# Kernel optimization log

Hardware: AMD Instinct MI355X
Metric: run time of the kernel (lower is better)

The kernel has to match this reference:

```python
import jax, jax.numpy as jnp
import numpy as np

N, R, E, H, D_MAX = 1024, 8192, 1024, 4, 48
DH = E // H
P_EDGE = 16.0 / R  # average in-degree ~16


def setup_inputs() -> dict:
    key = jax.random.key(0)
    ks = jax.random.split(key, 6)
    s = 0.02
    return {
        "target": jax.random.normal(ks[0], (N, E), jnp.float32),
        "source": jax.random.normal(ks[1], (R, E), jnp.float32),
        "adj": (jax.random.uniform(ks[2], (N, R)) < P_EDGE).astype(jnp.float32),
        "W_trans": jax.random.normal(ks[3], (E, E), jnp.float32) * s,
        "b_trans": jnp.zeros((E,), jnp.float32),
        "in_proj_w": jax.random.normal(ks[4], (3 * E, E), jnp.float32) * s,
        "in_proj_b": jnp.zeros((3 * E,), jnp.float32),
        "out_w": jax.random.normal(ks[5], (E, E), jnp.float32) * s,
        "out_b": jnp.zeros((E,), jnp.float32),
        "unit_id": 0,
    }


def reference(target, source, adj, W_trans, b_trans, in_proj_w, in_proj_b, out_w, out_b, unit_id):
    # source = relu(trans_fc(source))
    src = jax.nn.relu(source @ W_trans.T + b_trans)  # [R, E]

    # build padded neighbor index lists (torch loops per node; here vectorized)
    deg = adj.sum(axis=1).astype(jnp.int32)                # [N]
    order = jnp.argsort(-adj, axis=1)[:, :D_MAX]           # stable: 1-columns first, ascending col idx
    valid = jnp.arange(D_MAX)[None, :] < deg[:, None]      # [N, D] True = real neighbor
    neigh = jnp.where(valid, order, 0)                     # pad with index 0 (masked, like torch)
    kv_in = src[neigh]                                     # [N, D, E] gathered neighbor feats

    # nn.MultiheadAttention: q=target (len-1 query), k=v=padded neighbors
    Wq, Wk, Wv = jnp.split(in_proj_w, 3, axis=0)
    bq, bk, bv = jnp.split(in_proj_b, 3)
    q = (target @ Wq.T + bq).reshape(-1, H, DH)            # [N, H, dh]
    k = (kv_in @ Wk.T + bk).reshape(-1, D_MAX, H, DH)      # [N, D, H, dh]
    v = (kv_in @ Wv.T + bv).reshape(-1, D_MAX, H, DH)

    scores = jnp.einsum('nhd,nkhd->nhk', q, k) / np.float32(np.sqrt(DH))  # [N, H, D]
    # key_padding_mask: padded slots -> -inf; give zero-degree nodes one dummy
    # unmasked slot so softmax stays finite (their output is zeroed below)
    safe_valid = valid.at[:, 0].set(valid[:, 0] | (deg == 0))
    scores = jnp.where(safe_valid[:, None, :], scores, -jnp.inf)
    attn = jax.nn.softmax(scores, axis=-1)
    out = jnp.einsum('nhk,nkhd->nhd', attn, v).reshape(-1, E)
    out = out @ out_w.T + out_b

    # scatter back: inactive (degree-0) nodes stay zero, like att_res_padded
    return jnp.where((deg > 0)[:, None], out, jnp.zeros((), out.dtype))
```

## Files before the change

### kernel.cpp

```cpp
#include <hip/hip_runtime.h>

#define N_NODES 1024
#define R_SRC   8192
#define E_DIM   1024
#define H_HEADS 4
#define DH_DIM  256
#define D_MAXN  48
#define NCONVB  1024

typedef __attribute__((ext_vector_type(8))) short short8;
typedef __attribute__((ext_vector_type(4))) float f32x4;

__device__ __forceinline__ unsigned short f2bf(float f) {
    unsigned u = __float_as_uint(f);
    unsigned r = u + 0x7fffu + ((u >> 16) & 1u);
    return (unsigned short)(r >> 16);
}
__device__ __forceinline__ float bf2f(unsigned short b) {
    return __uint_as_float(((unsigned)b) << 16);
}
__device__ __forceinline__ void gload16(const void* g, void* l) {
    __builtin_amdgcn_global_load_lds(
        (const __attribute__((address_space(1))) unsigned int*)g,
        (__attribute__((address_space(3))) unsigned int*)l,
        16, 0, 0);
}
template<int N> __device__ __forceinline__ void vwait() {
    if constexpr (N == 8)       asm volatile("s_waitcnt vmcnt(8)" ::: "memory");
    else if constexpr (N == 6)  asm volatile("s_waitcnt vmcnt(6)" ::: "memory");
    else if constexpr (N == 4)  asm volatile("s_waitcnt vmcnt(4)" ::: "memory");
    else if constexpr (N == 2)  asm volatile("s_waitcnt vmcnt(2)" ::: "memory");
    else                        asm volatile("s_waitcnt vmcnt(0)" ::: "memory");
}

struct GD {
    const unsigned short* A;
    const unsigned short* B;
    const float* bias;
    void* C;
    int N, K, nbx, relu, outbf;
    const int* rowmask;
};

template<int BM, int BN>
__global__ __launch_bounds__(512) void gemm_t(GD d0, GD d1, int split)
{
    constexpr int AI = BM / 64;
    constexpr int BI = BN / 64;
    constexpr int VN = AI + BI;
    constexpr int FM = BM / 32;
    constexpr int FN = BN / 64;

    __shared__ __align__(16) unsigned short lds[3][(BM + BN) * 64];

    int bid = blockIdx.x;
    const int nwg = gridDim.x;
    bid = (bid & 7) * (nwg >> 3) + (bid >> 3);

    GD d; int q;
    if (bid < split) { d = d0; q = bid; }
    else             { d = d1; q = bid - split; }
    const int m0 = (q / d.nbx) * BM;
    const int n0 = (q % d.nbx) * BN;
    const int K  = d.K;

    const int t = threadIdx.x;
    const int w = t >> 6, l = t & 63;
    const int wm = w >> 2, wn = w & 3;

    const int trow = t >> 3, tkc = t & 7;
    const int tswz = tkc ^ (trow & 7);
    const unsigned short* gA[AI];
    const unsigned short* gB[BI];
#pragma unroll
    for (int i = 0; i < AI; ++i)
        gA[i] = d.A + (size_t)(m0 + i * 64 + trow) * K + tswz * 8;
#pragma unroll
    for (int i = 0; i < BI; ++i)
        gB[i] = d.B + (size_t)(n0 + i * 64 + trow) * K + tswz * 8;

    f32x4 acc[FM][FN] = {};

    auto STAGE = [&](int c, int kt) {
        const int ko = kt * 64;
#pragma unroll
        for (int i = 0; i < AI; ++i)
            gload16(gA[i] + ko, &lds[c][(i * 512 + t) * 8]);
#pragma unroll
        for (int i = 0; i < BI; ++i)
            gload16(gB[i] + ko, &lds[c][BM * 64 + (i * 512 + t) * 8]);
    };

    const int nt = K / 64;
    STAGE(0, 0);
    STAGE(1, 1);
    vwait<VN>();
    __builtin_amdgcn_s_barrier();

    const int lr = l & 15, hi = l >> 4;
    const int rsw = l & 7;
    const int cs0 = ((0 + hi) ^ rsw) * 8;
    const int cs1 = ((4 + hi) ^ rsw) * 8;
    const int abase = (wm * (BM / 2) + lr) * 64;
    const int bbase = BM * 64 + (wn * 64 + lr) * 64;

    for (int kt = 0; kt < nt; ++kt) {
        const int cur = kt % 3;
        if (kt + 2 < nt) STAGE((kt + 2) % 3, kt + 2);

        const unsigned short* Ls = &lds[cur][0];

        short8 bv[FN][2];
#pragma unroll
        for (int fj = 0; fj < FN; ++fj) {
            bv[fj][0] = *(const short8*)&Ls[bbase + fj * 1024 + cs0];
            bv[fj][1] = *(const short8*)&Ls[bbase + fj * 1024 + cs1];
        }
#pragma unroll
        for (int g = 0; g < FM; g += 4) {
            short8 av[4][2];
#pragma unroll
            for (int fi = 0; fi < 4; ++fi) {
                av[fi][0] = *(const short8*)&Ls[abase + (g + fi) * 1024 + cs0];
                av[fi][1] = *(const short8*)&Ls[abase + (g + fi) * 1024 + cs1];
            }
            __builtin_amdgcn_s_setprio(1);
#pragma unroll
            for (int ks = 0; ks < 2; ++ks)
#pragma unroll
                for (int fi = 0; fi < 4; ++fi)
#pragma unroll
                    for (int fj = 0; fj < FN; ++fj)
                        acc[g + fi][fj] = __builtin_amdgcn_mfma_f32_16x16x32_bf16(
                            av[fi][ks], bv[fj][ks], acc[g + fi][fj], 0, 0, 0);
            __builtin_amdgcn_s_setprio(0);
        }

        asm volatile("" ::: "memory");
        __builtin_amdgcn_s_barrier();
        if (kt + 2 < nt) {
            vwait<VN>();
        } else {
            vwait<0>();
        }
        __builtin_amdgcn_s_barrier();
    }

#pragma unroll
    for (int fj = 0; fj < FN; ++fj) {
        const int c = n0 + wn * 64 + fj * 16 + lr;
        const float bvs = d.bias[c];
#pragma unroll
        for (int fi = 0; fi < FM; ++fi) {
            const int rb = m0 + wm * (BM / 2) + fi * 16 + hi * 4;
#pragma unroll
            for (int qq = 0; qq < 4; ++qq) {
                const int r = rb + qq;
                float x = acc[fi][fj][qq] + bvs;
                if (d.relu) x = fmaxf(x, 0.0f);
                if (d.rowmask && d.rowmask[r] == 0) x = 0.0f;
                if (d.outbf) ((unsigned short*)d.C)[(size_t)r * d.N + c] = f2bf(x);
                else         ((float*)d.C)[(size_t)r * d.N + c] = x;
            }
        }
    }
}

struct GS {
    const unsigned short* A;
    const unsigned short* B;
    const float* bias;
    void* C;
    int lda, ldb, ldc, K, relu, outbf;
    long long azs, bzs, czs;
    int bias_zs;
    const int* rowmask;
};

__global__ __launch_bounds__(256) void gemm_s(GS g)
{
    const int z = blockIdx.z;
    const unsigned short* A = g.A + (size_t)((long long)z * g.azs);
    const unsigned short* B = g.B + (size_t)((long long)z * g.bzs);
    const float* bias = g.bias ? g.bias + (size_t)z * g.bias_zs : nullptr;

    __shared__ __align__(16) unsigned short S[3][128 * 32];

    const int t = threadIdx.x;
    const int m0 = blockIdx.y * 64;
    const int n0 = blockIdx.x * 64;
    const int w = t >> 6, l = t & 63;
    const int wrow = (w >> 1) * 32;
    const int wcol = (w & 1) * 32;
    const int lr = l & 15;
    const int kg = (l >> 4) * 8;

    f32x4 acc[2][2] = {};

    const unsigned short* gp0 = A + (size_t)(m0 + (t >> 2)) * g.lda + (t & 3) * 8;
    const unsigned short* gp1 = B + (size_t)(n0 + (t >> 2)) * g.ldb + (t & 3) * 8;

    auto STAGE = [&](int c, int k0) {
        gload16(gp0 + k0, &S[c][t * 8]);
        gload16(gp1 + k0, &S[c][2048 + t * 8]);
    };

    const int nt = g.K / 32;
    STAGE(0, 0);
    STAGE(1, 32);
    vwait<2>();
    __builtin_amdgcn_s_barrier();

    for (int kt = 0; kt < nt; ++kt) {
        const int cur = kt % 3;
        if (kt + 2 < nt) STAGE((kt + 2) % 3, (kt + 2) * 32);

        const unsigned short* Ls = &S[cur][0];

        short8 af[2], bw[2];
#pragma unroll
        for (int i = 0; i < 2; ++i)
            af[i] = *(const short8*)&Ls[(wrow + i * 16 + lr) * 32 + kg];
#pragma unroll
        for (int j = 0; j < 2; ++j)
            bw[j] = *(const short8*)&Ls[2048 + (wcol + j * 16 + lr) * 32 + kg];
#pragma unroll
        for (int i = 0; i < 2; ++i)
#pragma unroll
            for (int j = 0; j < 2; ++j)
                acc[i][j] = __builtin_amdgcn_mfma_f32_16x16x32_bf16(
                    af[i], bw[j], acc[i][j], 0, 0, 0);

        asm volatile("" ::: "memory");
        __builtin_amdgcn_s_barrier();
        if (kt + 2 < nt) {
            vwait<2>();
        } else {
            vwait<0>();
        }
        __builtin_amdgcn_s_barrier();
    }

#pragma unroll
    for (int j = 0; j < 2; ++j) {
        const int c = n0 + wcol + j * 16 + lr;
        const float bv = bias ? bias[c] : 0.0f;
#pragma unroll
        for (int i = 0; i < 2; ++i) {
            const int rbase = m0 + wrow + i * 16 + (l >> 4) * 4;
#pragma unroll
            for (int qq = 0; qq < 4; ++qq) {
                const int r = rbase + qq;
                float x = acc[i][j][qq] + bv;
                if (g.relu) x = fmaxf(x, 0.0f);
                if (g.rowmask && g.rowmask[r] == 0) x = 0.0f;
                if (g.outbf)
                    ((unsigned short*)g.C)[(size_t)((long long)z * g.czs) + (size_t)r * g.ldc + c] = f2bf(x);
                else
                    ((float*)g.C)[(size_t)((long long)z * g.czs) + (size_t)r * g.ldc + c] = x;
            }
        }
    }
}

struct ConvArgs {
    const float* s[4];
    unsigned short* d[4];
    unsigned off[5];
};

__global__ __launch_bounds__(256) void pre_kernel(
    const float* __restrict__ adj, int* __restrict__ neigh, int* __restrict__ deg,
    ConvArgs a, const float* __restrict__ inw_f, const float* __restrict__ tgt_f,
    const float* __restrict__ in_b, unsigned short* __restrict__ WkT,
    unsigned short* __restrict__ Q_bf)
{
    __shared__ __align__(16) unsigned char smem[64 * 65 * 4];
    const int t = threadIdx.x;

    if (blockIdx.x < 256) {
        unsigned short (*QS)[64 * 32] = (unsigned short (*)[64 * 32])smem;
        const int qb = blockIdx.x;
        const int m0 = (qb >> 4) * 64;
        const int n0 = (qb & 15) * 64;
        const int w = t >> 6, l = t & 63;
        const int wrow = (w >> 1) * 32;
        const int wcol = (w & 1) * 32;
        const int lr = l & 15;
        const int kg = (l >> 4) * 8;
        const int row = t >> 2, k8 = (t & 3) * 8;

        const float* ga = tgt_f + (size_t)(m0 + row) * E_DIM + k8;
        const float* gb = inw_f + (size_t)(n0 + row) * E_DIM + k8;

        f32x4 acc[2][2] = {};

        for (int k0 = 0; k0 < E_DIM; k0 += 32) {
            float4 a0 = *(const float4*)(ga + k0);
            float4 a1 = *(const float4*)(ga + k0 + 4);
            float4 b0 = *(const float4*)(gb + k0);
            float4 b1 = *(const float4*)(gb + k0 + 4);
            short8 av, bv;
            av[0] = (short)f2bf(a0.x); av[1] = (short)f2bf(a0.y);
            av[2] = (short)f2bf(a0.z); av[3] = (short)f2bf(a0.w);
            av[4] = (short)f2bf(a1.x); av[5] = (short)f2bf(a1.y);
            av[6] = (short)f2bf(a1.z); av[7] = (short)f2bf(a1.w);
            bv[0] = (short)f2bf(b0.x); bv[1] = (short)f2bf(b0.y);
            bv[2] = (short)f2bf(b0.z); bv[3] = (short)f2bf(b0.w);
            bv[4] = (short)f2bf(b1.x); bv[5] = (short)f2bf(b1.y);
            bv[6] = (short)f2bf(b1.z); bv[7] = (short)f2bf(b1.w);
            *(short8*)&QS[0][row * 32 + k8] = av;
            *(short8*)&QS[1][row * 32 + k8] = bv;
            __syncthreads();

            short8 af[2], bw[2];
#pragma unroll
            for (int i = 0; i < 2; ++i)
                af[i] = *(const short8*)&QS[0][(wrow + i * 16 + lr) * 32 + kg];
#pragma unroll
            for (int j = 0; j < 2; ++j)
                bw[j] = *(const short8*)&QS[1][(wcol + j * 16 + lr) * 32 + kg];
#pragma unroll
            for (int i = 0; i < 2; ++i)
#pragma unroll
                for (int j = 0; j < 2; ++j)
                    acc[i][j] = __builtin_amdgcn_mfma_f32_16x16x32_bf16(
                        af[i], bw[j], acc[i][j], 0, 0, 0);
            __syncthreads();
        }

#pragma unroll
        for (int j = 0; j < 2; ++j) {
            const int c = n0 + wcol + j * 16 + lr;
            const float bv = in_b[c];
#pragma unroll
            for (int i = 0; i < 2; ++i) {
                const int rbase = m0 + wrow + i * 16 + (l >> 4) * 4;
#pragma unroll
                for (int qq = 0; qq < 4; ++qq)
                    Q_bf[(size_t)(rbase + qq) * E_DIM + c] = f2bf(acc[i][j][qq] + bv);
            }
        }
        return;
    }

    if (blockIdx.x < 512) {
        float (*tile)[65] = (float (*)[65])smem;
        const int tb = blockIdx.x - 256;
        const int h = tb >> 6, rem = tb & 63;
        const int e0 = (rem >> 2) * 64, d0 = (rem & 3) * 64;
        const int r = t >> 2, c4 = (t & 3) * 16;
        const float* tsrc = inw_f + (size_t)(E_DIM + h * 256 + d0 + r) * E_DIM + e0 + c4;
#pragma unroll
        for (int jj = 0; jj < 4; ++jj) {
            float4 v = ((const float4*)tsrc)[jj];
            tile[r][c4 + jj * 4 + 0] = v.x;
            tile[r][c4 + jj * 4 + 1] = v.y;
            tile[r][c4 + jj * 4 + 2] = v.z;
            tile[r][c4 + jj * 4 + 3] = v.w;
        }
        __syncthreads();
        const int er = t >> 2, dc = (t & 3) * 16;
        unsigned short* wout = WkT + ((size_t)h * E_DIM + e0 + er) * 256 + d0 + dc;
#pragma unroll
        for (int jj = 0; jj < 4; ++jj) {
            ushort4 o;
            o.x = f2bf(tile[dc + jj * 4 + 0][er]);
            o.y = f2bf(tile[dc + jj * 4 + 1][er]);
            o.z = f2bf(tile[dc + jj * 4 + 2][er]);
            o.w = f2bf(tile[dc + jj * 4 + 3][er]);
            ((ushort4*)wout)[jj] = o;
        }
        return;
    }

    if (blockIdx.x < (unsigned)(512 + N_NODES)) {
        int* s_cnt = (int*)smem;
        int (*s_idx)[D_MAXN] = (int (*)[D_MAXN])(smem + 16);

        const int n    = blockIdx.x - 512;
        const int w    = t >> 6;
        const int lane = t & 63;
        const float* row = adj + (size_t)n * R_SRC;

        const int seg0 = w * (R_SRC / 4);
        const unsigned long long lower = (1ULL << lane) - 1ULL;
        int total = 0;

        for (int base = seg0; base < seg0 + R_SRC / 4; base += 256) {
            const float v0 = row[base + lane];
            const float v1 = row[base + 64 + lane];
            const float v2 = row[base + 128 + lane];
            const float v3 = row[base + 192 + lane];
            const unsigned long long m0 = __ballot(v0 != 0.0f);
            const unsigned long long m1 = __ballot(v1 != 0.0f);
            const unsigned long long m2 = __ballot(v2 != 0.0f);
            const unsigned long long m3 = __ballot(v3 != 0.0f);
            int p;
            p = total + __popcll(m0 & lower);
            if (v0 != 0.0f && p < D_MAXN) s_idx[w][p] = base + lane;
            total += __popcll(m0);
            p = total + __popcll(m1 & lower);
            if (v1 != 0.0f && p < D_MAXN) s_idx[w][p] = base + 64 + lane;
            total += __popcll(m1);
            p = total + __popcll(m2 & lower);
            if (v2 != 0.0f && p < D_MAXN) s_idx[w][p] = base + 128 + lane;
            total += __popcll(m2);
            p = total + __popcll(m3 & lower);
            if (v3 != 0.0f && p < D_MAXN) s_idx[w][p] = base + 192 + lane;
            total += __popcll(m3);
        }
        if (lane == 0) s_cnt[w] = total;
        __syncthreads();

        int start = 0;
#pragma unroll
        for (int i = 0; i < 4; ++i) if (i < w) start += s_cnt[i];
        const int degree = s_cnt[0] + s_cnt[1] + s_cnt[2] + s_cnt[3];
        const int nstore = total < D_MAXN ? total : D_MAXN;
        if (lane < nstore) {
            const int gpos = start + lane;
            if (gpos < D_MAXN) neigh[n * D_MAXN + gpos] = s_idx[w][lane];
        }
        if (t == 0) deg[n] = degree;
        return;
    }

    {
        const unsigned total = a.off[4];
        const unsigned stride = NCONVB * 1024;
        for (unsigned bs = (blockIdx.x - 512 - N_NODES) * 1024; bs < total; bs += stride) {
            float4 v[4];
            unsigned idx[4];
            int ok[4];
#pragma unroll
            for (int j = 0; j < 4; ++j) {
                idx[j] = bs + j * 256 + t;
                ok[j] = idx[j] < total;
            }
            int seg[4];
#pragma unroll
            for (int j = 0; j < 4; ++j) {
                seg[j] = 0;
#pragma unroll
                for (int s = 1; s < 4; ++s) seg[j] += (idx[j] >= a.off[s]);
            }
#pragma unroll
            for (int j = 0; j < 4; ++j)
                if (ok[j]) v[j] = ((const float4*)a.s[seg[j]])[idx[j] - a.off[seg[j]]];
#pragma unroll
            for (int j = 0; j < 4; ++j) {
                if (ok[j]) {
                    ushort4 o;
                    o.x = f2bf(v[j].x); o.y = f2bf(v[j].y);
                    o.z = f2bf(v[j].z); o.w = f2bf(v[j].w);
                    ((ushort4*)a.d[seg[j]])[idx[j] - a.off[seg[j]]] = o;
                }
            }
        }
    }
}

__global__ __launch_bounds__(256) void gather_ctx(
    const float* __restrict__ Ahat, const unsigned short* __restrict__ srcrel,
    const int* __restrict__ neigh, const int* __restrict__ deg,
    unsigned short* __restrict__ ctx)
{
    const int n = blockIdx.x;
    const int t = threadIdx.x;
    const int h = t >> 6;
    const int lane = t & 63;

    unsigned short* crow = ctx + ((size_t)n * H_HEADS + h) * E_DIM + lane * 16;
    const int degree = deg[n];
    if (degree == 0) {
        ushort4 z4 = {0, 0, 0, 0};
#pragma unroll
        for (int j = 0; j < 4; ++j) ((ushort4*)crow)[j] = z4;
        return;
    }
    const int dv = degree < D_MAXN ? degree : D_MAXN;

    __shared__ int s_neigh[D_MAXN];
    if (t < dv) s_neigh[t] = neigh[n * D_MAXN + t];
    __syncthreads();

    float a[16];
    {
        const float4* ap = (const float4*)(Ahat + (size_t)n * (H_HEADS * E_DIM) + h * E_DIM + lane * 16);
#pragma unroll
        for (int j = 0; j < 4; ++j) {
            float4 v = ap[j];
            a[j * 4 + 0] = v.x; a[j * 4 + 1] = v.y; a[j * 4 + 2] = v.z; a[j * 4 + 3] = v.w;
        }
    }

    float m = -3.4e38f, sum = 0.0f;
    float cacc[16];
#pragma unroll
    for (int i = 0; i < 16; ++i) cacc[i] = 0.0f;

    const float scale = 0.0625f;

    int d = 0;
    for (; d + 1 < dv; d += 2) {
        const ushort4* rp0 = (const ushort4*)(srcrel + (size_t)s_neigh[d]     * E_DIM + lane * 16);
        const ushort4* rp1 = (const ushort4*)(srcrel + (size_t)s_neigh[d + 1] * E_DIM + lane * 16);
        ushort4 w00 = rp0[0], w01 = rp0[1], w02 = rp0[2], w03 = rp0[3];
        ushort4 w10 = rp1[0], w11 = rp1[1], w12 = rp1[2], w13 = rp1[3];
        float e0[16], e1[16];
        e0[0]=bf2f(w00.x); e0[1]=bf2f(w00.y); e0[2]=bf2f(w00.z); e0[3]=bf2f(w00.w);
        e0[4]=bf2f(w01.x); e0[5]=bf2f(w01.y); e0[6]=bf2f(w01.z); e0[7]=bf2f(w01.w);
        e0[8]=bf2f(w02.x); e0[9]=bf2f(w02.y); e0[10]=bf2f(w02.z); e0[11]=bf2f(w02.w);
        e0[12]=bf2f(w03.x); e0[13]=bf2f(w03.y); e0[14]=bf2f(w03.z); e0[15]=bf2f(w03.w);
        e1[0]=bf2f(w10.x); e1[1]=bf2f(w10.y); e1[2]=bf2f(w10.z); e1[3]=bf2f(w10.w);
        e1[4]=bf2f(w11.x); e1[5]=bf2f(w11.y); e1[6]=bf2f(w11.z); e1[7]=bf2f(w11.w);
        e1[8]=bf2f(w12.x); e1[9]=bf2f(w12.y); e1[10]=bf2f(w12.z); e1[11]=bf2f(w12.w);
        e1[12]=bf2f(w13.x); e1[13]=bf2f(w13.y); e1[14]=bf2f(w13.z); e1[15]=bf2f(w13.w);

        float s0 = 0.0f, s1 = 0.0f;
#pragma unroll
        for (int i = 0; i < 16; ++i) { s0 = fmaf(a[i], e0[i], s0); s1 = fmaf(a[i], e1[i], s1); }
#pragma unroll
        for (int off = 32; off > 0; off >>= 1) {
            s0 += __shfl_xor(s0, off);
            s1 += __shfl_xor(s1, off);
        }
        s0 *= scale; s1 *= scale;

        if (s0 > m) {
            const float f = __expf(m - s0);
            sum *= f;
#pragma unroll
            for (int i = 0; i < 16; ++i) cacc[i] *= f;
            m = s0;
        }
        {
            const float wgt = __expf(s0 - m);
            sum += wgt;
#pragma unroll
            for (int i = 0; i < 16; ++i) cacc[i] = fmaf(wgt, e0[i], cacc[i]);
        }
        if (s1 > m) {
            const float f = __expf(m - s1);
            sum *= f;
#pragma unroll
            for (int i = 0; i < 16; ++i) cacc[i] *= f;
            m = s1;
        }
        {
            const float wgt = __expf(s1 - m);
            sum += wgt;
#pragma unroll
            for (int i = 0; i < 16; ++i) cacc[i] = fmaf(wgt, e1[i], cacc[i]);
        }
    }
    for (; d < dv; ++d) {
        const ushort4* rp = (const ushort4*)(srcrel + (size_t)s_neigh[d] * E_DIM + lane * 16);
        float e[16];
#pragma unroll
        for (int j = 0; j < 4; ++j) {
            ushort4 v = rp[j];
            e[j * 4 + 0] = bf2f(v.x); e[j * 4 + 1] = bf2f(v.y);
            e[j * 4 + 2] = bf2f(v.z); e[j * 4 + 3] = bf2f(v.w);
        }
        float s = 0.0f;
#pragma unroll
        for (int i = 0; i < 16; ++i) s = fmaf(a[i], e[i], s);
#pragma unroll
        for (int off = 32; off > 0; off >>= 1) s += __shfl_xor(s, off);
        s *= scale;
        if (s > m) {
            const float f = __expf(m - s);
            sum *= f;
#pragma unroll
            for (int i = 0; i < 16; ++i) cacc[i] *= f;
            m = s;
        }
        const float wgt = __expf(s - m);
        sum += wgt;
#pragma unroll
        for (int i = 0; i < 16; ++i) cacc[i] = fmaf(wgt, e[i], cacc[i]);
    }

    const float inv = 1.0f / sum;
#pragma unroll
    for (int j = 0; j < 4; ++j) {
        ushort4 o;
        o.x = f2bf(cacc[j * 4 + 0] * inv);
        o.y = f2bf(cacc[j * 4 + 1] * inv);
        o.z = f2bf(cacc[j * 4 + 2] * inv);
        o.w = f2bf(cacc[j * 4 + 3] * inv);
        ((ushort4*)crow)[j] = o;
    }
}

extern "C" void kernel_launch(void* const* d_in, const int* in_sizes, int n_in,
                              void* d_out, int out_size, void* d_ws, size_t ws_size,
                              hipStream_t stream)
{
    const float* target  = (const float*)d_in[0];
    const float* source  = (const float*)d_in[1];
    const float* adj     = (const float*)d_in[2];
    const float* W_trans = (const float*)d_in[3];
    const float* b_trans = (const float*)d_in[4];
    const float* in_w    = (const float*)d_in[5];
    const float* in_b    = (const float*)d_in[6];
    const float* out_w   = (const float*)d_in[7];
    const float* out_b   = (const float*)d_in[8];
    float* out = (float*)d_out;

    char* ws = (char*)d_ws;
    unsigned short* src_bf    = (unsigned short*)ws; ws += (size_t)R_SRC * E_DIM * 2;
    unsigned short* wt_bf     = (unsigned short*)ws; ws += (size_t)E_DIM * E_DIM * 2;
    unsigned short* wv_bf     = (unsigned short*)ws; ws += (size_t)E_DIM * E_DIM * 2;
    unsigned short* outw_bf   = (unsigned short*)ws; ws += (size_t)E_DIM * E_DIM * 2;
    unsigned short* srcrel_bf = (unsigned short*)ws; ws += (size_t)R_SRC * E_DIM * 2;
    unsigned short* WkT_bf    = (unsigned short*)ws; ws += (size_t)H_HEADS * E_DIM * DH_DIM * 2;
    unsigned short* Q_bf      = (unsigned short*)ws; ws += (size_t)N_NODES * E_DIM * 2;
    float*          Ahat      = (float*)ws;         ws += (size_t)N_NODES * H_HEADS * E_DIM * 4;
    unsigned short* ctx_bf    = (unsigned short*)ws; ws += (size_t)N_NODES * H_HEADS * E_DIM * 2;
    unsigned short* attn_bf   = (unsigned short*)ws; ws += (size_t)N_NODES * E_DIM * 2;
    int*            neigh     = (int*)ws;            ws += (size_t)N_NODES * D_MAXN * 4;
    int*            deg       = (int*)ws;            ws += (size_t)N_NODES * 4;

    const size_t EE = (size_t)E_DIM * E_DIM;

    {
        ConvArgs a;
        const unsigned sz4[4] = {
            (unsigned)((size_t)R_SRC * E_DIM / 4),
            (unsigned)(EE / 4),
            (unsigned)(EE / 4),
            (unsigned)(EE / 4)};
        a.s[0] = source;        a.d[0] = src_bf;
        a.s[1] = W_trans;       a.d[1] = wt_bf;
        a.s[2] = in_w + 2 * EE; a.d[2] = wv_bf;
        a.s[3] = out_w;         a.d[3] = outw_bf;
        a.off[0] = 0;
        for (int i = 0; i < 4; ++i) a.off[i + 1] = a.off[i] + sz4[i];
        pre_kernel<<<512 + N_NODES + NCONVB, 256, 0, stream>>>(
            adj, neigh, deg, a, in_w, target, in_b, WkT_bf, Q_bf);
    }

    {
        GD ds;
        ds.A = src_bf; ds.B = wt_bf; ds.bias = b_trans; ds.C = srcrel_bf;
        ds.N = E_DIM; ds.K = E_DIM; ds.nbx = E_DIM / 256; ds.relu = 1; ds.outbf = 1;
        ds.rowmask = nullptr;
        const int sblocks = (R_SRC / 128) * (E_DIM / 256);
        gemm_t<128, 256><<<sblocks, 512, 0, stream>>>(ds, ds, sblocks);
    }

    {
        GS g;
        g.A = Q_bf; g.B = WkT_bf; g.bias = nullptr; g.C = Ahat;
        g.lda = E_DIM; g.ldb = DH_DIM; g.ldc = H_HEADS * E_DIM; g.K = DH_DIM;
        g.relu = 0; g.outbf = 0;
        g.azs = DH_DIM;
        g.bzs = (long long)E_DIM * DH_DIM;
        g.czs = E_DIM;
        g.bias_zs = 0; g.rowmask = nullptr;
        gemm_s<<<dim3(E_DIM / 64, N_NODES / 64, H_HEADS), 256, 0, stream>>>(g);
    }

    gather_ctx<<<N_NODES, 256, 0, stream>>>(Ahat, srcrel_bf, neigh, deg, ctx_bf);

    {
        GS g;
        g.A = ctx_bf; g.B = wv_bf; g.bias = in_b + 2 * E_DIM; g.C = attn_bf;
        g.lda = H_HEADS * E_DIM; g.ldb = E_DIM; g.ldc = E_DIM; g.K = E_DIM;
        g.relu = 0; g.outbf = 1;
        g.azs = E_DIM;
        g.bzs = (long long)DH_DIM * E_DIM;
        g.czs = DH_DIM;
        g.bias_zs = DH_DIM; g.rowmask = nullptr;
        gemm_s<<<dim3(DH_DIM / 64, N_NODES / 64, H_HEADS), 256, 0, stream>>>(g);
    }

    {
        GS g;
        g.A = attn_bf; g.B = outw_bf; g.bias = out_b; g.C = out;
        g.lda = E_DIM; g.ldb = E_DIM; g.ldc = E_DIM; g.K = E_DIM;
        g.relu = 0; g.outbf = 0; g.azs = 0; g.bzs = 0; g.czs = 0; g.bias_zs = 0;
        g.rowmask = deg;
        gemm_s<<<dim3(E_DIM / 64, N_NODES / 64, 1), 256, 0, stream>>>(g);
    }
}
```

Baseline: 105.9 us.

## Precompute per-head Wk^T Wq product and apply target directly to it

Replaces the Q projection GEMM inside pre_kernel with a weight-only product M_h = Wk_h^T Wq_h, plus a bias term bqk = Wk_h^T bq. Ahat is then computed as target times M_h in one K=1024 GEMM per head, and target is converted to bf16 in the conversion pass. This removes the in-kernel Q GEMM from the preprocessing launch. In exchange it adds a 4x1024x1024x256 weight GEMM and raises the Ahat GEMM's K from 256 to 1024, so total FLOPs grow. Rounding M to bf16 also changes the numerics.

```diff
diff --git a/kernel.cpp b/kernel.cpp
--- a/kernel.cpp
+++ b/kernel.cpp
@@ -264,93 +264,29 @@
 }
 
 struct ConvArgs {
-    const float* s[4];
-    unsigned short* d[4];
-    unsigned off[5];
+    const float* s[5];
+    unsigned short* d[5];
+    unsigned off[6];
 };
 
 __global__ __launch_bounds__(256) void pre_kernel(
     const float* __restrict__ adj, int* __restrict__ neigh, int* __restrict__ deg,
-    ConvArgs a, const float* __restrict__ inw_f, const float* __restrict__ tgt_f,
-    const float* __restrict__ in_b, unsigned short* __restrict__ WkT,
-    unsigned short* __restrict__ Q_bf)
+    ConvArgs a, const float* __restrict__ inw_f, const float* __restrict__ in_b,
+    unsigned short* __restrict__ WkT, unsigned short* __restrict__ WqT,
+    float* __restrict__ bqk)
 {
     __shared__ __align__(16) unsigned char smem[64 * 65 * 4];
     const int t = threadIdx.x;
 
-    if (blockIdx.x < 256) {
-        unsigned short (*QS)[64 * 32] = (unsigned short (*)[64 * 32])smem;
-        const int qb = blockIdx.x;
-        const int m0 = (qb >> 4) * 64;
-        const int n0 = (qb & 15) * 64;
-        const int w = t >> 6, l = t & 63;
-        const int wrow = (w >> 1) * 32;
-        const int wcol = (w & 1) * 32;
-        const int lr = l & 15;
-        const int kg = (l >> 4) * 8;
-        const int row = t >> 2, k8 = (t & 3) * 8;
-
-        const float* ga = tgt_f + (size_t)(m0 + row) * E_DIM + k8;
-        const float* gb = inw_f + (size_t)(n0 + row) * E_DIM + k8;
-
-        f32x4 acc[2][2] = {};
-
-        for (int k0 = 0; k0 < E_DIM; k0 += 32) {
-            float4 a0 = *(const float4*)(ga + k0);
-            float4 a1 = *(const float4*)(ga + k0 + 4);
-            float4 b0 = *(const float4*)(gb + k0);
-            float4 b1 = *(const float4*)(gb + k0 + 4);
-            short8 av, bv;
-            av[0] = (short)f2bf(a0.x); av[1] = (short)f2bf(a0.y);
-            av[2] = (short)f2bf(a0.z); av[3] = (short)f2bf(a0.w);
-            av[4] = (short)f2bf(a1.x); av[5] = (short)f2bf(a1.y);
-            av[6] = (short)f2bf(a1.z); av[7] = (short)f2bf(a1.w);
-            bv[0] = (short)f2bf(b0.x); bv[1] = (short)f2bf(b0.y);
-            bv[2] = (short)f2bf(b0.z); bv[3] = (short)f2bf(b0.w);
-            bv[4] = (short)f2bf(b1.x); bv[5] = (short)f2bf(b1.y);
-            bv[6] = (short)f2bf(b1.z); bv[7] = (short)f2bf(b1.w);
-            *(short8*)&QS[0][row * 32 + k8] = av;
-            *(short8*)&QS[1][row * 32 + k8] = bv;
-            __syncthreads();
-
-            short8 af[2], bw[2];
-#pragma unroll
-            for (int i = 0; i < 2; ++i)
-                af[i] = *(const short8*)&QS[0][(wrow + i * 16 + lr) * 32 + kg];
-#pragma unroll
-            for (int j = 0; j < 2; ++j)
-                bw[j] = *(const short8*)&QS[1][(wcol + j * 16 + lr) * 32 + kg];
-#pragma unroll
-            for (int i = 0; i < 2; ++i)
-#pragma unroll
-                for (int j = 0; j < 2; ++j)
-                    acc[i][j] = __builtin_amdgcn_mfma_f32_16x16x32_bf16(
-                        af[i], bw[j], acc[i][j], 0, 0, 0);
-            __syncthreads();
-        }
-
-#pragma unroll
-        for (int j = 0; j < 2; ++j) {
-            const int c = n0 + wcol + j * 16 + lr;
-            const float bv = in_b[c];
-#pragma unroll
-            for (int i = 0; i < 2; ++i) {
-                const int rbase = m0 + wrow + i * 16 + (l >> 4) * 4;
-#pragma unroll
-                for (int qq = 0; qq < 4; ++qq)
-                    Q_bf[(size_t)(rbase + qq) * E_DIM + c] = f2bf(acc[i][j][qq] + bv);
-            }
-        }
-        return;
-    }
-
     if (blockIdx.x < 512) {
         float (*tile)[65] = (float (*)[65])smem;
-        const int tb = blockIdx.x - 256;
-        const int h = tb >> 6, rem = tb & 63;
+        const int is_k = blockIdx.x < 256;
+        const int sub = blockIdx.x & 255;
+        const int h = sub >> 6, rem = sub & 63;
         const int e0 = (rem >> 2) * 64, d0 = (rem & 3) * 64;
+        const int rowbase = (is_k ? E_DIM : 0) + h * 256 + d0;
         const int r = t >> 2, c4 = (t & 3) * 16;
-        const float* tsrc = inw_f + (size_t)(E_DIM + h * 256 + d0 + r) * E_DIM + e0 + c4;
+        const float* tsrc = inw_f + (size_t)(rowbase + r) * E_DIM + e0 + c4;
 #pragma unroll
         for (int jj = 0; jj < 4; ++jj) {
             float4 v = ((const float4*)tsrc)[jj];
@@ -361,7 +297,8 @@
         }
         __syncthreads();
         const int er = t >> 2, dc = (t & 3) * 16;
-        unsigned short* wout = WkT + ((size_t)h * E_DIM + e0 + er) * 256 + d0 + dc;
+        unsigned short* wout = (is_k ? WkT : WqT)
+            + ((size_t)h * E_DIM + e0 + er) * 256 + d0 + dc;
 #pragma unroll
         for (int jj = 0; jj < 4; ++jj) {
             ushort4 o;
@@ -374,11 +311,27 @@
         return;
     }
 
-    if (blockIdx.x < (unsigned)(512 + N_NODES)) {
+    if (blockIdx.x < 516) {
+        const int h = blockIdx.x - 512;
+        float acc[4] = {0.f, 0.f, 0.f, 0.f};
+#pragma unroll 4
+        for (int dd = 0; dd < 256; ++dd) {
+            const float bv = in_b[h * 256 + dd];
+            const float* row = inw_f + (size_t)(E_DIM + h * 256 + dd) * E_DIM;
+#pragma unroll
+            for (int j = 0; j < 4; ++j)
+                acc[j] = fmaf(bv, row[t + j * 256], acc[j]);
+        }
+#pragma unroll
+        for (int j = 0; j < 4; ++j) bqk[h * E_DIM + t + j * 256] = acc[j];
+        return;
+    }
+
+    if (blockIdx.x < (unsigned)(516 + N_NODES)) {
         int* s_cnt = (int*)smem;
         int (*s_idx)[D_MAXN] = (int (*)[D_MAXN])(smem + 16);
 
-        const int n    = blockIdx.x - 512;
+        const int n    = blockIdx.x - 516;
         const int w    = t >> 6;
         const int lane = t & 63;
         const float* row = adj + (size_t)n * R_SRC;
@@ -427,9 +380,9 @@
     }
 
     {
-        const unsigned total = a.off[4];
+        const unsigned total = a.off[5];
         const unsigned stride = NCONVB * 1024;
-        for (unsigned bs = (blockIdx.x - 512 - N_NODES) * 1024; bs < total; bs += stride) {
+        for (unsigned bs = (blockIdx.x - 516 - N_NODES) * 1024; bs < total; bs += stride) {
             float4 v[4];
             unsigned idx[4];
             int ok[4];
@@ -443,7 +396,7 @@
             for (int j = 0; j < 4; ++j) {
                 seg[j] = 0;
 #pragma unroll
-                for (int s = 1; s < 4; ++s) seg[j] += (idx[j] >= a.off[s]);
+                for (int s = 1; s < 5; ++s) seg[j] += (idx[j] >= a.off[s]);
             }
 #pragma unroll
             for (int j = 0; j < 4; ++j)
@@ -615,10 +568,13 @@
     unsigned short* wt_bf     = (unsigned short*)ws; ws += (size_t)E_DIM * E_DIM * 2;
     unsigned short* wv_bf     = (unsigned short*)ws; ws += (size_t)E_DIM * E_DIM * 2;
     unsigned short* outw_bf   = (unsigned short*)ws; ws += (size_t)E_DIM * E_DIM * 2;
+    unsigned short* tgt_bf    = (unsigned short*)ws; ws += (size_t)N_NODES * E_DIM * 2;
     unsigned short* srcrel_bf = (unsigned short*)ws; ws += (size_t)R_SRC * E_DIM * 2;
     unsigned short* WkT_bf    = (unsigned short*)ws; ws += (size_t)H_HEADS * E_DIM * DH_DIM * 2;
-    unsigned short* Q_bf      = (unsigned short*)ws; ws += (size_t)N_NODES * E_DIM * 2;
-    float*          Ahat      = (float*)ws;         ws += (size_t)N_NODES * H_HEADS * E_DIM * 4;
+    unsigned short* WqT_bf    = (unsigned short*)ws; ws += (size_t)H_HEADS * E_DIM * DH_DIM * 2;
+    unsigned short* M_bf      = (unsigned short*)ws; ws += (size_t)H_HEADS * E_DIM * E_DIM * 2;
+    float*          bqk       = (float*)ws;          ws += (size_t)H_HEADS * E_DIM * 4;
+    float*          Ahat      = (float*)ws;          ws += (size_t)N_NODES * H_HEADS * E_DIM * 4;
     unsigned short* ctx_bf    = (unsigned short*)ws; ws += (size_t)N_NODES * H_HEADS * E_DIM * 2;
     unsigned short* attn_bf   = (unsigned short*)ws; ws += (size_t)N_NODES * E_DIM * 2;
     int*            neigh     = (int*)ws;            ws += (size_t)N_NODES * D_MAXN * 4;
@@ -628,19 +584,21 @@
 
     {
         ConvArgs a;
-        const unsigned sz4[4] = {
+        const unsigned sz4[5] = {
             (unsigned)((size_t)R_SRC * E_DIM / 4),
             (unsigned)(EE / 4),
             (unsigned)(EE / 4),
-            (unsigned)(EE / 4)};
+            (unsigned)(EE / 4),
+            (unsigned)((size_t)N_NODES * E_DIM / 4)};
         a.s[0] = source;        a.d[0] = src_bf;
         a.s[1] = W_trans;       a.d[1] = wt_bf;
         a.s[2] = in_w + 2 * EE; a.d[2] = wv_bf;
         a.s[3] = out_w;         a.d[3] = outw_bf;
+        a.s[4] = target;        a.d[4] = tgt_bf;
         a.off[0] = 0;
-        for (int i = 0; i < 4; ++i) a.off[i + 1] = a.off[i] + sz4[i];
-        pre_kernel<<<512 + N_NODES + NCONVB, 256, 0, stream>>>(
-            adj, neigh, deg, a, in_w, target, in_b, WkT_bf, Q_bf);
+        for (int i = 0; i < 5; ++i) a.off[i + 1] = a.off[i] + sz4[i];
+        pre_kernel<<<516 + N_NODES + NCONVB, 256, 0, stream>>>(
+            adj, neigh, deg, a, in_w, in_b, WkT_bf, WqT_bf, bqk);
     }
 
     {
@@ -654,13 +612,25 @@
 
     {
         GS g;
-        g.A = Q_bf; g.B = WkT_bf; g.bias = nullptr; g.C = Ahat;
-        g.lda = E_DIM; g.ldb = DH_DIM; g.ldc = H_HEADS * E_DIM; g.K = DH_DIM;
+        g.A = WkT_bf; g.B = WqT_bf; g.bias = nullptr; g.C = M_bf;
+        g.lda = DH_DIM; g.ldb = DH_DIM; g.ldc = E_DIM; g.K = DH_DIM;
+        g.relu = 0; g.outbf = 1;
+        g.azs = (long long)E_DIM * DH_DIM;
+        g.bzs = (long long)E_DIM * DH_DIM;
+        g.czs = (long long)E_DIM * E_DIM;
+        g.bias_zs = 0; g.rowmask = nullptr;
+        gemm_s<<<dim3(E_DIM / 64, E_DIM / 64, H_HEADS), 256, 0, stream>>>(g);
+    }
+
+    {
+        GS g;
+        g.A = tgt_bf; g.B = M_bf; g.bias = bqk; g.C = Ahat;
+        g.lda = E_DIM; g.ldb = E_DIM; g.ldc = H_HEADS * E_DIM; g.K = E_DIM;
         g.relu = 0; g.outbf = 0;
-        g.azs = DH_DIM;
-        g.bzs = (long long)E_DIM * DH_DIM;
+        g.azs = 0;
+        g.bzs = (long long)E_DIM * E_DIM;
         g.czs = E_DIM;
-        g.bias_zs = 0; g.rowmask = nullptr;
+        g.bias_zs = E_DIM; g.rowmask = nullptr;
         gemm_s<<<dim3(E_DIM / 64, N_NODES / 64, H_HEADS), 256, 0, stream>>>(g);
     }
 
```

Result: slower. 134.5 us (+27.0%).
